# Optimization experiments

Hardware: AMD Instinct MI355X
Metric: run time of the kernel (lower is better)

Reference implementation:

```python
import jax, jax.numpy as jnp
import numpy as np

NUM_LEVELS = 16
LEVEL_DIM = 2
BASE_RES = 16
MAX_RES = 2048
LOG2_T = 21
TABLE_SIZE = 1 << LOG2_T
HASH_MASK = TABLE_SIZE - 1
BBOX_SCALE = 2.0
N_POINTS = 262144

# per-level integer resolutions, exactly as int(np.floor(base * b**i))
_b = np.exp((np.log(MAX_RES) - np.log(BASE_RES)) / (NUM_LEVELS - 1))
RESOLUTIONS = np.array([int(np.floor(BASE_RES * _b ** i)) for i in range(NUM_LEVELS)], dtype=np.float32)

PRIMES = np.array([73856093, 19349663, 83492791], dtype=np.int32)
# 8 corner offsets of the unit cube, same order as the torch module
OFFSETS = np.array([[0, 0, 0], [0, 0, 1], [0, 1, 0], [0, 1, 1],
                    [1, 0, 0], [1, 0, 1], [1, 1, 0], [1, 1, 1]], dtype=np.int32)


def setup_inputs() -> dict:
    key = jax.random.key(0)
    kx, kt = jax.random.split(key)
    x = jax.random.normal(kx, (N_POINTS, 3), dtype=jnp.float32)
    # nn.init.uniform_(w, a=-1e-4, b=1e-4) for each level, stacked
    tables = jax.random.uniform(kt, (NUM_LEVELS, TABLE_SIZE, LEVEL_DIM),
                                dtype=jnp.float32, minval=-1e-4, maxval=1e-4)
    return {"x": x, "tables": tables}


def reference(x, tables):
    # x: [N,3]; tables: [L,T,D]
    res = jnp.asarray(RESOLUTIONS)                      # [L]
    primes = jnp.asarray(PRIMES)                        # [3]
    offsets = jnp.asarray(OFFSETS)                      # [8,3]

    x_norm = jnp.clip((x + BBOX_SCALE) / (2 * BBOX_SCALE), 0.0, 1.0)   # [N,3]
    scaled = x_norm[None, :, :] * res[:, None, None]    # [L,N,3]
    x0 = jnp.floor(scaled).astype(jnp.int32)            # [L,N,3] (non-negative)
    w = scaled - x0.astype(jnp.float32)                 # [L,N,3] trilinear fractions

    # all 8 corners at once: [L,N,8,3]
    corners = x0[:, :, None, :] + offsets[None, None, :, :]
    # spatial hash: xor of coord*prime; low 21 bits are identical whether
    # computed in int64 (torch) or wrapping int32, since we mask to 2^21.
    cp = corners * primes                                # [L,N,8,3] int32 (wraps)
    idx = (cp[..., 0] ^ cp[..., 1] ^ cp[..., 2]) & HASH_MASK   # [L,N,8]

    # per-level gather: [L,N,8,D]
    emb = jax.vmap(lambda t, i: t[i])(tables, idx)

    # trilinear weights: prod_k (offset_k ? w_k : 1-w_k) -> [L,N,8]
    wc = jnp.where(offsets[None, None, :, :] == 0,
                   1.0 - w[:, :, None, :], w[:, :, None, :]).prod(axis=-1)

    feat = jnp.einsum('lnc,lncd->lnd', wc, emb)          # [L,N,D]
    # torch.cat(features, dim=-1): level-major along last dim
    out = jnp.transpose(feat, (1, 0, 2)).reshape(x.shape[0], NUM_LEVELS * LEVEL_DIM)
    return out
```

## Files before the change

### kernel.cpp

```cpp
#include <hip/hip_runtime.h>
#include <math.h>

#define NUM_LEVELS 16
#define LOG2_T 21
#define TABLE_SIZE (1u << LOG2_T)
#define HASH_MASK (TABLE_SIZE - 1u)
#define N_POINTS 262144
#define GRID_P1 1024
#define PTS_PER_BLOCK 2048
#define PX 73856093u
#define PY 19349663u
#define PZ 83492791u

struct Args { float r[NUM_LEVELS]; int l2nc[NUM_LEVELS]; };

#define CAT3_(a, b, c) a##b##c
#define TREG(SET, i) CAT3_(t, SET, i)

#define CORNER(SET, i)                                                        \
    {                                                                         \
        const uint32_t h = (((i) & 4) ? X1 : X0) ^ (((i) & 2) ? Y1 : Y0)      \
                         ^ (((i) & 1) ? Z1 : Z0);                             \
        const uint32_t idx = h & HASH_MASK;                                   \
        const bool m = (idx >> shift) == (uint32_t)c;                         \
        const uint32_t off = m ? (idx << 3) : dummy_off;                      \
        wc##SET[i] = m ? (((((i) & 4) ? qx : axq) * (((i) & 2) ? qy : ayq))   \
                          * (((i) & 1) ? qz : azq))                           \
                       : 0.0f;                                                \
        asm volatile("global_load_dwordx2 %0, %1, %2"                         \
                     : "=v"(TREG(SET, i)) : "v"(off), "s"(tab));              \
    }

#define ISSUE(SET, p)                                                         \
    {                                                                         \
        const float sx = nxx[p] * r, sy = nyy[p] * r, sz = nzz[p] * r;        \
        const float fx = floorf(sx), fy = floorf(sy), fz = floorf(sz);        \
        const float qx = sx - fx, qy = sy - fy, qz = sz - fz;                 \
        const float axq = 1.0f - qx, ayq = 1.0f - qy, azq = 1.0f - qz;        \
        const uint32_t X0 = (uint32_t)(int)fx * PX;                           \
        const uint32_t Y0 = (uint32_t)(int)fy * PY;                           \
        const uint32_t Z0 = (uint32_t)(int)fz * PZ;                           \
        const uint32_t X1 = X0 + PX, Y1 = Y0 + PY, Z1 = Z0 + PZ;              \
        CORNER(SET, 0) CORNER(SET, 1) CORNER(SET, 2) CORNER(SET, 3)           \
        CORNER(SET, 4) CORNER(SET, 5) CORNER(SET, 6) CORNER(SET, 7)           \
    }

#define WAIT(SET, CNT)                                                        \
    asm volatile("s_waitcnt vmcnt(" #CNT ")"                                  \
                 : "+v"(TREG(SET, 0)), "+v"(TREG(SET, 1)),                    \
                   "+v"(TREG(SET, 2)), "+v"(TREG(SET, 3)),                    \
                   "+v"(TREG(SET, 4)), "+v"(TREG(SET, 5)),                    \
                   "+v"(TREG(SET, 6)), "+v"(TREG(SET, 7)));

#define FMA2(SET, p, i)                                                       \
    a0[p] = fmaf(wc##SET[i], TREG(SET, i).x, a0[p]);                          \
    a1[p] = fmaf(wc##SET[i], TREG(SET, i).y, a1[p]);

#define FMA8(SET, p)                                                          \
    FMA2(SET, p, 0) FMA2(SET, p, 1) FMA2(SET, p, 2) FMA2(SET, p, 3)           \
    FMA2(SET, p, 4) FMA2(SET, p, 5) FMA2(SET, p, 6) FMA2(SET, p, 7)

__global__ __launch_bounds__(256) void hash_embed_phase1_v12(
    const float* __restrict__ x,
    const float* __restrict__ tables,
    float2* __restrict__ wsbuf,
    Args args)
{
    const int bid = blockIdx.x;
    const int slot = bid & 7;
    const int slice = bid >> 3;
    const int base = slice * PTS_PER_BLOCK + threadIdx.x;

    float nxx[8], nyy[8], nzz[8];
    #pragma unroll
    for (int p = 0; p < 8; ++p) {
        const int n = base + p * 256;
        const float px = x[n * 3 + 0];
        const float py = x[n * 3 + 1];
        const float pz = x[n * 3 + 2];
        nxx[p] = fminf(fmaxf((px + 2.0f) * 0.25f, 0.0f), 1.0f);
        nyy[p] = fminf(fmaxf((py + 2.0f) * 0.25f, 0.0f), 1.0f);
        nzz[p] = fminf(fmaxf((pz + 2.0f) * 0.25f, 0.0f), 1.0f);
    }

    #pragma unroll 1
    for (int li = 0; li < 2; ++li) {
        const int lv = (li == 0) ? slot : 15 - slot;
        const float r = args.r[lv];
        const int l2nc = args.l2nc[lv];
        const int shift = LOG2_T - l2nc;
        const int nc = 1 << l2nc;
        const float* __restrict__ tab =
            tables + (size_t)lv * ((size_t)TABLE_SIZE * 2);

        float a0[8], a1[8];
        #pragma unroll
        for (int p = 0; p < 8; ++p) { a0[p] = 0.0f; a1[p] = 0.0f; }

        #pragma unroll 1
        for (int c = 0; c < nc; ++c) {
            const uint32_t dummy_off = ((uint32_t)c << shift) << 3;
            float2 tA0, tA1, tA2, tA3, tA4, tA5, tA6, tA7;
            float2 tB0, tB1, tB2, tB3, tB4, tB5, tB6, tB7;
            float wcA[8], wcB[8];

            ISSUE(A, 0)
            ISSUE(B, 1) WAIT(A, 8) FMA8(A, 0)
            ISSUE(A, 2) WAIT(B, 8) FMA8(B, 1)
            ISSUE(B, 3) WAIT(A, 8) FMA8(A, 2)
            ISSUE(A, 4) WAIT(B, 8) FMA8(B, 3)
            ISSUE(B, 5) WAIT(A, 8) FMA8(A, 4)
            ISSUE(A, 6) WAIT(B, 8) FMA8(B, 5)
            ISSUE(B, 7) WAIT(A, 8) FMA8(A, 6)
                        WAIT(B, 0) FMA8(B, 7)
        }

        #pragma unroll
        for (int p = 0; p < 8; ++p) {
            wsbuf[(size_t)lv * N_POINTS + base + p * 256] = make_float2(a0[p], a1[p]);
        }
    }
}

__global__ __launch_bounds__(256) void hash_embed_phase2(
    const float2* __restrict__ ws,
    float2* __restrict__ out)
{
    __shared__ float2 tile[64][NUM_LEVELS + 1];
    const int n0 = blockIdx.x * 64;
    const int t = threadIdx.x;
    #pragma unroll
    for (int k = 0; k < 4; ++k) {
        const int e = k * 256 + t;
        const int l = e >> 6;
        const int j = e & 63;
        tile[j][l] = ws[(size_t)l * N_POINTS + n0 + j];
    }
    __syncthreads();
    #pragma unroll
    for (int k = 0; k < 4; ++k) {
        const int e = k * 256 + t;
        const int nl = e >> 4;
        const int l = e & 15;
        out[(size_t)(n0 + nl) * NUM_LEVELS + l] = tile[nl][l];
    }
}

__global__ __launch_bounds__(256) void hash_embed_direct(
    const float* __restrict__ x,
    const float* __restrict__ tables,
    float* __restrict__ out,
    Args args)
{
    const int t = blockIdx.x * blockDim.x + threadIdx.x;
    const int n = t >> 4;
    const int l = t & 15;
    if (n >= N_POINTS) return;

    const float px = x[n * 3 + 0];
    const float py = x[n * 3 + 1];
    const float pz = x[n * 3 + 2];
    const float nx = fminf(fmaxf((px + 2.0f) * 0.25f, 0.0f), 1.0f);
    const float ny = fminf(fmaxf((py + 2.0f) * 0.25f, 0.0f), 1.0f);
    const float nz = fminf(fmaxf((pz + 2.0f) * 0.25f, 0.0f), 1.0f);

    const float r = args.r[l];
    const float sx = nx * r, sy = ny * r, sz = nz * r;
    const float fx = floorf(sx), fy = floorf(sy), fz = floorf(sz);
    const float wxv = sx - fx, wyv = sy - fy, wzv = sz - fz;

    const uint32_t hx0 = (uint32_t)(int)fx * PX;
    const uint32_t hy0 = (uint32_t)(int)fy * PY;
    const uint32_t hz0 = (uint32_t)(int)fz * PZ;
    const uint32_t hx1 = hx0 + PX, hy1 = hy0 + PY, hz1 = hz0 + PZ;

    const float ax = 1.0f - wxv, ay = 1.0f - wyv, az = 1.0f - wzv;
    const float* __restrict__ tab = tables + (size_t)l * ((size_t)TABLE_SIZE * 2);

    float f0 = 0.0f, f1 = 0.0f;
    #pragma unroll
    for (int c = 0; c < 8; ++c) {
        const uint32_t hh = ((c & 4) ? hx1 : hx0) ^ ((c & 2) ? hy1 : hy0)
                          ^ ((c & 1) ? hz1 : hz0);
        const uint32_t idx = hh & HASH_MASK;
        const float2 emb = *reinterpret_cast<const float2*>(tab + (size_t)idx * 2);
        const float w = (((c & 4) ? wxv : ax) * ((c & 2) ? wyv : ay)) * ((c & 1) ? wzv : az);
        f0 = fmaf(w, emb.x, f0);
        f1 = fmaf(w, emb.y, f1);
    }
    float2* o = reinterpret_cast<float2*>(out + (size_t)n * (NUM_LEVELS * 2) + l * 2);
    *o = make_float2(f0, f1);
}

extern "C" void kernel_launch(void* const* d_in, const int* in_sizes, int n_in,
                              void* d_out, int out_size, void* d_ws, size_t ws_size,
                              hipStream_t stream) {
    const float* x      = (const float*)d_in[0];
    const float* tables = (const float*)d_in[1];
    float* out          = (float*)d_out;

    Args args;
    const double b = exp((log(2048.0) - log(16.0)) / 15.0);
    for (int i = 0; i < NUM_LEVELS; ++i) {
        const double ri = floor(16.0 * pow(b, (double)i));
        args.r[i] = (float)ri;
        double E = (ri + 1.0) * (ri + 1.0) * (ri + 1.0);
        if (E > 1.8e6) E = 1.8e6;
        const double lines = 262144.0 * (1.0 - exp(-8.0 * E / 2097152.0));
        const double bytes = lines * 64.0;
        int l2 = 0;
        while (l2 < 3 && bytes / (double)(1 << l2) > 3.7e6) ++l2;
        args.l2nc[i] = l2;
    }

    const size_t ws_needed = (size_t)NUM_LEVELS * N_POINTS * sizeof(float2);
    if (ws_size >= ws_needed) {
        float2* wsbuf = (float2*)d_ws;
        hipLaunchKernelGGL(hash_embed_phase1_v12, dim3(GRID_P1), dim3(256),
                           0, stream, x, tables, wsbuf, args);
        hipLaunchKernelGGL(hash_embed_phase2, dim3(N_POINTS / 64), dim3(256),
                           0, stream, wsbuf, (float2*)out);
    } else {
        const int total = N_POINTS * NUM_LEVELS;
        hipLaunchKernelGGL(hash_embed_direct, dim3((total + 255) / 256), dim3(256),
                           0, stream, x, tables, out, args);
    }
}
```

Baseline: 229.5 us.

## Balance phase-1 work via flat list of level-chunk units with atomic accumulation

Replaces the fixed two-levels-per-slot assignment with a host-built list of (level, chunk) work units spread evenly across the 8 slots. Chunk counts per level are now arbitrary integers up to 8, and chunk ids come from a multiply-shift instead of a power-of-two shift. Because a level's chunks may fall in different slots, partial sums go to a zero-initialized workspace through atomicAdd. The aim is to remove load imbalance between slots, at the cost of an extra memset and atomic traffic.

```diff
diff --git a/kernel.cpp b/kernel.cpp
--- a/kernel.cpp
+++ b/kernel.cpp
@@ -1,5 +1,6 @@
 #include <hip/hip_runtime.h>
 #include <math.h>
+#include <string.h>
 
 #define NUM_LEVELS 16
 #define LOG2_T 21
@@ -8,11 +9,17 @@
 #define N_POINTS 262144
 #define GRID_P1 1024
 #define PTS_PER_BLOCK 2048
+#define MAX_UNITS 128
 #define PX 73856093u
 #define PY 19349663u
 #define PZ 83492791u
 
-struct Args { float r[NUM_LEVELS]; int l2nc[NUM_LEVELS]; };
+struct Args {
+    float r[NUM_LEVELS];
+    uint32_t ncMul[NUM_LEVELS];
+    uint32_t units[MAX_UNITS];
+    int slotStart[9];
+};
 
 #define CAT3_(a, b, c) a##b##c
 #define TREG(SET, i) CAT3_(t, SET, i)
@@ -22,7 +29,8 @@
         const uint32_t h = (((i) & 4) ? X1 : X0) ^ (((i) & 2) ? Y1 : Y0)      \
                          ^ (((i) & 1) ? Z1 : Z0);                             \
         const uint32_t idx = h & HASH_MASK;                                   \
-        const bool m = (idx >> shift) == (uint32_t)c;                         \
+        const uint32_t cid = (idx * ncMul) >> 21;                             \
+        const bool m = (cid == cc);                                           \
         const uint32_t off = m ? (idx << 3) : dummy_off;                      \
         wc##SET[i] = m ? (((((i) & 4) ? qx : axq) * (((i) & 2) ? qy : ayq))   \
                           * (((i) & 1) ? qz : azq))                           \
@@ -60,10 +68,10 @@
     FMA2(SET, p, 0) FMA2(SET, p, 1) FMA2(SET, p, 2) FMA2(SET, p, 3)           \
     FMA2(SET, p, 4) FMA2(SET, p, 5) FMA2(SET, p, 6) FMA2(SET, p, 7)
 
-__global__ __launch_bounds__(256) void hash_embed_phase1_v12(
+__global__ __launch_bounds__(256) void hash_embed_phase1_v15(
     const float* __restrict__ x,
     const float* __restrict__ tables,
-    float2* __restrict__ wsbuf,
+    float* __restrict__ wsbuf,
     Args args)
 {
     const int bid = blockIdx.x;
@@ -75,49 +83,64 @@
     #pragma unroll
     for (int p = 0; p < 8; ++p) {
         const int n = base + p * 256;
-        const float px = x[n * 3 + 0];
-        const float py = x[n * 3 + 1];
-        const float pz = x[n * 3 + 2];
-        nxx[p] = fminf(fmaxf((px + 2.0f) * 0.25f, 0.0f), 1.0f);
-        nyy[p] = fminf(fmaxf((py + 2.0f) * 0.25f, 0.0f), 1.0f);
-        nzz[p] = fminf(fmaxf((pz + 2.0f) * 0.25f, 0.0f), 1.0f);
-    }
+        nxx[p] = fminf(fmaxf((x[n*3+0] + 2.0f) * 0.25f, 0.0f), 1.0f);
+        nyy[p] = fminf(fmaxf((x[n*3+1] + 2.0f) * 0.25f, 0.0f), 1.0f);
+        nzz[p] = fminf(fmaxf((x[n*3+2] + 2.0f) * 0.25f, 0.0f), 1.0f);
+    }
+
+    float a0[8], a1[8];
+    int curLv = -1;
+
+    const int ubeg = args.slotStart[slot];
+    const int uend = args.slotStart[slot + 1];
 
     #pragma unroll 1
-    for (int li = 0; li < 2; ++li) {
-        const int lv = (li == 0) ? slot : 15 - slot;
+    for (int uu = ubeg; uu < uend; ++uu) {
+        const uint32_t u = args.units[uu];
+        const int lv = (int)(u >> 27);
+        const uint32_t cc = (u >> 24) & 7u;
+        const uint32_t dummy_off = (u & 0xFFFFFFu) << 3;
+
+        if (lv != curLv) {
+            if (curLv >= 0) {
+                #pragma unroll
+                for (int p = 0; p < 8; ++p) {
+                    float* w = wsbuf + ((size_t)curLv * N_POINTS + base + p*256) * 2;
+                    atomicAdd(w,     a0[p]);
+                    atomicAdd(w + 1, a1[p]);
+                }
+            }
+            curLv = lv;
+            #pragma unroll
+            for (int p = 0; p < 8; ++p) { a0[p] = 0.0f; a1[p] = 0.0f; }
+        }
+
         const float r = args.r[lv];
-        const int l2nc = args.l2nc[lv];
-        const int shift = LOG2_T - l2nc;
-        const int nc = 1 << l2nc;
+        const uint32_t ncMul = args.ncMul[lv];
         const float* __restrict__ tab =
             tables + (size_t)lv * ((size_t)TABLE_SIZE * 2);
 
-        float a0[8], a1[8];
-        #pragma unroll
-        for (int p = 0; p < 8; ++p) { a0[p] = 0.0f; a1[p] = 0.0f; }
-
-        #pragma unroll 1
-        for (int c = 0; c < nc; ++c) {
-            const uint32_t dummy_off = ((uint32_t)c << shift) << 3;
-            float2 tA0, tA1, tA2, tA3, tA4, tA5, tA6, tA7;
-            float2 tB0, tB1, tB2, tB3, tB4, tB5, tB6, tB7;
-            float wcA[8], wcB[8];
-
-            ISSUE(A, 0)
-            ISSUE(B, 1) WAIT(A, 8) FMA8(A, 0)
-            ISSUE(A, 2) WAIT(B, 8) FMA8(B, 1)
-            ISSUE(B, 3) WAIT(A, 8) FMA8(A, 2)
-            ISSUE(A, 4) WAIT(B, 8) FMA8(B, 3)
-            ISSUE(B, 5) WAIT(A, 8) FMA8(A, 4)
-            ISSUE(A, 6) WAIT(B, 8) FMA8(B, 5)
-            ISSUE(B, 7) WAIT(A, 8) FMA8(A, 6)
-                        WAIT(B, 0) FMA8(B, 7)
-        }
-
+        float2 tA0, tA1, tA2, tA3, tA4, tA5, tA6, tA7;
+        float2 tB0, tB1, tB2, tB3, tB4, tB5, tB6, tB7;
+        float wcA[8], wcB[8];
+
+        ISSUE(A, 0)
+        ISSUE(B, 1) WAIT(A, 8) FMA8(A, 0)
+        ISSUE(A, 2) WAIT(B, 8) FMA8(B, 1)
+        ISSUE(B, 3) WAIT(A, 8) FMA8(A, 2)
+        ISSUE(A, 4) WAIT(B, 8) FMA8(B, 3)
+        ISSUE(B, 5) WAIT(A, 8) FMA8(A, 4)
+        ISSUE(A, 6) WAIT(B, 8) FMA8(B, 5)
+        ISSUE(B, 7) WAIT(A, 8) FMA8(A, 6)
+                    WAIT(B, 0) FMA8(B, 7)
+    }
+
+    if (curLv >= 0) {
         #pragma unroll
         for (int p = 0; p < 8; ++p) {
-            wsbuf[(size_t)lv * N_POINTS + base + p * 256] = make_float2(a0[p], a1[p]);
+            float* w = wsbuf + ((size_t)curLv * N_POINTS + base + p*256) * 2;
+            atomicAdd(w,     a0[p]);
+            atomicAdd(w + 1, a1[p]);
         }
     }
 }
@@ -200,7 +223,9 @@
     float* out          = (float*)d_out;
 
     Args args;
+    memset(&args, 0, sizeof(args));
     const double b = exp((log(2048.0) - log(16.0)) / 15.0);
+    int nc[NUM_LEVELS];
     for (int i = 0; i < NUM_LEVELS; ++i) {
         const double ri = floor(16.0 * pow(b, (double)i));
         args.r[i] = (float)ri;
@@ -208,21 +233,43 @@
         if (E > 1.8e6) E = 1.8e6;
         const double lines = 262144.0 * (1.0 - exp(-8.0 * E / 2097152.0));
         const double bytes = lines * 64.0;
-        int l2 = 0;
-        while (l2 < 3 && bytes / (double)(1 << l2) > 3.7e6) ++l2;
-        args.l2nc[i] = l2;
-    }
+        int n = (bytes <= 2.5e6) ? 1 : (int)ceil(bytes / 2.8e6);
+        if (n < 1) n = 1;
+        if (n > 8) n = 8;
+        nc[i] = n;
+        args.ncMul[i] = (uint32_t)n;
+    }
+
+    uint32_t allUnits[MAX_UNITS];
+    int total = 0;
+    for (int l = 0; l < NUM_LEVELS; ++l) {
+        for (int c = 0; c < nc[l]; ++c) {
+            const uint32_t cstart =
+                (uint32_t)((((unsigned long long)c << 21) + (unsigned)nc[l] - 1)
+                           / (unsigned)nc[l]);
+            allUnits[total++] = ((uint32_t)l << 27) | ((uint32_t)c << 24) | cstart;
+        }
+    }
+    const int qn = total / 8, rm = total % 8;
+    int off = 0;
+    for (int s = 0; s < 8; ++s) {
+        args.slotStart[s] = off;
+        off += qn + (s < rm ? 1 : 0);
+    }
+    args.slotStart[8] = off;
+    for (int i = 0; i < total; ++i) args.units[i] = allUnits[i];
 
     const size_t ws_needed = (size_t)NUM_LEVELS * N_POINTS * sizeof(float2);
     if (ws_size >= ws_needed) {
-        float2* wsbuf = (float2*)d_ws;
-        hipLaunchKernelGGL(hash_embed_phase1_v12, dim3(GRID_P1), dim3(256),
+        float* wsbuf = (float*)d_ws;
+        hipMemsetAsync(d_ws, 0, ws_needed, stream);
+        hipLaunchKernelGGL(hash_embed_phase1_v15, dim3(GRID_P1), dim3(256),
                            0, stream, x, tables, wsbuf, args);
         hipLaunchKernelGGL(hash_embed_phase2, dim3(N_POINTS / 64), dim3(256),
-                           0, stream, wsbuf, (float2*)out);
+                           0, stream, (const float2*)wsbuf, (float2*)out);
     } else {
-        const int total = N_POINTS * NUM_LEVELS;
-        hipLaunchKernelGGL(hash_embed_direct, dim3((total + 255) / 256), dim3(256),
+        const int totalThreads = N_POINTS * NUM_LEVELS;
+        hipLaunchKernelGGL(hash_embed_direct, dim3((totalThreads + 255) / 256), dim3(256),
                            0, stream, x, tables, out, args);
     }
 }
```

New measurement: 461.6 us. 101% more time.
